# Optimization experiments

Hardware: AMD Instinct MI355X
Metric: run time of the kernel (lower is better)

Reference implementation:

```python
import jax, jax.numpy as jnp
import numpy as np

B, T, C, H = 4, 2048, 1024, 16
HD = C // H  # head dim = 64


def setup_inputs() -> dict:
    key = jax.random.key(0)
    k1, k2, k3 = jax.random.split(key, 3)
    scale_in = 1.0 / np.sqrt(C)
    return {
        "x": jax.random.normal(k1, (B, T, C), dtype=jnp.float32),
        "W_attn": jax.random.normal(k2, (C, 3 * C), dtype=jnp.float32) * scale_in,
        "b_attn": jnp.zeros((3 * C,), dtype=jnp.float32),
        "W_proj": jax.random.normal(k3, (C, C), dtype=jnp.float32) * scale_in,
        "b_proj": jnp.zeros((C,), dtype=jnp.float32),
    }


def reference(x, W_attn, b_attn, W_proj, b_proj):
    b, t, c = x.shape
    qkv = x @ W_attn + b_attn                      # [B,T,3C]
    q, k, v = jnp.split(qkv, 3, axis=-1)
    # [B,T,C] -> [B,H,T,HD]
    def heads(z):
        return z.reshape(b, t, H, HD).transpose(0, 2, 1, 3)
    q, k, v = heads(q), heads(k), heads(v)
    att = jnp.einsum("bhqd,bhkd->bhqk", q, k) / jnp.sqrt(jnp.float32(HD))
    causal = jnp.tril(jnp.ones((t, t), dtype=bool))
    att = jnp.where(causal, att, -jnp.inf)
    att = jax.nn.softmax(att, axis=-1)             # dropout p=0 -> identity
    y = jnp.einsum("bhqk,bhkd->bhqd", att, v)      # [B,H,T,HD]
    y = y.transpose(0, 2, 1, 3).reshape(b, t, c)   # [B,T,C]
    return y @ W_proj + b_proj
```

## Files before the change

kernel.cpp:

```cpp
#include <hip/hip_runtime.h>
#include <hip/hip_bf16.h>

typedef unsigned int u32;
typedef unsigned short u16;
typedef __bf16 bf16x8 __attribute__((ext_vector_type(8)));
typedef float f32x4 __attribute__((ext_vector_type(4)));
typedef _Float16 f16;
typedef _Float16 f16x2 __attribute__((ext_vector_type(2)));
typedef _Float16 f16x4 __attribute__((ext_vector_type(4)));
typedef _Float16 f16x8 __attribute__((ext_vector_type(8)));

#define B_ 4
#define T_ 2048
#define C_ 1024
#define H_ 16
#define HD_ 64
#define M_ (B_*T_)
#define N3C (3*C_)
#define N2C (2*C_)

__device__ __forceinline__ u16 f2bf(float f) {
  u32 u = __builtin_bit_cast(u32, f);
  u = (u + 0x7fffu + ((u >> 16) & 1u)) >> 16;
  return (u16)u;
}

#define GLD16(gp, lp) __builtin_amdgcn_global_load_lds( \
    (const __attribute__((address_space(1))) u32*)(gp), \
    (__attribute__((address_space(3))) u32*)(lp), 16, 0, 0)

#if __has_builtin(__builtin_amdgcn_exp2f)
#define EXP2F(x) __builtin_amdgcn_exp2f(x)
#else
#define EXP2F(x) exp2f(x)
#endif

template<int N> __device__ __forceinline__ void vmw() {
  if constexpr (N == 0)      asm volatile("s_waitcnt vmcnt(0)" ::: "memory");
  else if constexpr (N == 3) asm volatile("s_waitcnt vmcnt(3)" ::: "memory");
  else if constexpr (N == 4) asm volatile("s_waitcnt vmcnt(4)" ::: "memory");
  else if constexpr (N == 6) asm volatile("s_waitcnt vmcnt(6)" ::: "memory");
  else                       asm volatile("s_waitcnt vmcnt(8)" ::: "memory");
}

__global__ __launch_bounds__(256) void prep(
    const float* __restrict__ x, const float* __restrict__ Wa,
    const float* __restrict__ Wp,
    u16* __restrict__ xb, u16* __restrict__ W1t, u16* __restrict__ W2t) {
  __shared__ float t[32][33];
  const int blk = blockIdx.x, tid = threadIdx.x;
  if (blk < 8192) {
    int i = blk * 256 + tid;
    float4 v = ((const float4*)x)[i];
    ushort4 o;
    o.x = f2bf(v.x); o.y = f2bf(v.y); o.z = f2bf(v.z); o.w = f2bf(v.w);
    ((ushort4*)xb)[i] = o;
    return;
  }
  const float* W; u16* Wt; int Ndim, id;
  if (blk < 8192 + 3072) { W = Wa; Wt = W1t; Ndim = N3C; id = blk - 8192; }
  else                   { W = Wp; Wt = W2t; Ndim = C_;  id = blk - 11264; }
  const int nt = Ndim / 32;
  const int n0 = (id % nt) * 32, k0 = (id / nt) * 32;
  const int tx = tid & 31, ty = tid >> 5;
  #pragma unroll
  for (int i = ty; i < 32; i += 8)
    t[i][tx] = W[(long)(k0 + i) * Ndim + n0 + tx];
  __syncthreads();
  #pragma unroll
  for (int i = ty; i < 32; i += 8)
    Wt[(long)(n0 + i) * C_ + k0 + tx] = f2bf(t[tx][i]);
}

template<int BM>
__device__ __forceinline__ void gemm_core32(
    const u16* __restrict__ A, const u16* __restrict__ Bt,
    u16* lds, long rowA0, long colB0, int tid, f32x4 acc[BM/32][4]) {
  constexpr int MT = BM / 32;
  constexpr int SA = BM / 128;
  constexpr int AEL = BM * 32;
  constexpr int SLOTE = (BM + 256) * 32;
  constexpr int VMAIN = 2 * (SA + 2);
  const int lane = tid & 63, wave = tid >> 6;
  const int wm = wave >> 2, wn = wave & 3;
  const int l15 = lane & 15, quad = lane >> 4;
  const int srow = tid >> 2;
  const int schunk = (tid & 3) ^ (srow & 3);
  const u16* Ag = A + (long)(rowA0 + srow) * C_ + (schunk << 3);
  const u16* Bg = Bt + (long)(colB0 + srow) * C_ + (schunk << 3);
  const int fsw = (quad ^ (l15 & 3)) << 3;
  const int aOff = (wm * (BM / 2) + l15) * 32 + fsw;
  const int bOff = AEL + (wn * 64 + l15) * 32 + fsw;

#define SLOTP(k) (lds + ((k) & 3) * SLOTE)
#define STA_(k, j) GLD16(Ag + (k) * 32 + (long)(j) * 128 * C_, \
                         SLOTP(k) + (j) * 4096 + tid * 8)
#define STB_(k, j) GLD16(Bg + (k) * 32 + (long)(j) * 128 * C_, \
                         SLOTP(k) + AEL + (j) * 4096 + tid * 8)
#define KTILE_(kt, SC, WC) do {                                              \
    const u16* sl_ = SLOTP(kt);                                              \
    SC;                                                                      \
    bf16x8 bfr[4], afr[MT];                                                  \
    _Pragma("unroll")                                                        \
    for (int n = 0; n < 4; ++n)                                              \
      bfr[n] = *(const bf16x8*)&sl_[bOff + n * 512];                         \
    _Pragma("unroll")                                                        \
    for (int m = 0; m < MT; ++m)                                             \
      afr[m] = *(const bf16x8*)&sl_[aOff + m * 512];                         \
    asm volatile("s_waitcnt lgkmcnt(0)" ::: "memory");                       \
    __builtin_amdgcn_sched_barrier(0);                                       \
    __builtin_amdgcn_s_setprio(1);                                           \
    _Pragma("unroll")                                                        \
    for (int m = 0; m < MT; ++m)                                             \
      _Pragma("unroll")                                                      \
      for (int n = 0; n < 4; ++n)                                            \
        acc[m][n] = __builtin_amdgcn_mfma_f32_16x16x32_bf16(                 \
            afr[m], bfr[n], acc[m][n], 0, 0, 0);                             \
    __builtin_amdgcn_s_setprio(0);                                           \
    WC;                                                                      \
    asm volatile("s_barrier" ::: "memory");                                  \
  } while (0)

  #pragma unroll
  for (int t = 0; t < 3; ++t) {
    STA_(t, 0); STB_(t, 0); STB_(t, 1);
    if constexpr (SA == 2) STA_(t, 1);
  }
  vmw<VMAIN>();
  asm volatile("s_barrier" ::: "memory");

  #pragma unroll
  for (int kt = 0; kt < 29; ++kt) {
    KTILE_(kt,
           { STA_(kt + 3, 0); STB_(kt + 3, 0); STB_(kt + 3, 1);
             if constexpr (SA == 2) STA_(kt + 3, 1); },
           (vmw<VMAIN>()));
  }
  KTILE_(29, , (vmw<VMAIN / 2>()));
  KTILE_(30, , (vmw<0>()));
  KTILE_(31, , );
#undef KTILE_
#undef STB_
#undef STA_
#undef SLOTP
}

__global__ __launch_bounds__(512, 2) void gemm_qkv(
    const u16* __restrict__ A, const u16* __restrict__ Bt,
    const float* __restrict__ bias, u16* __restrict__ qkout,
    f16* __restrict__ vt) {
  __shared__ u16 lds[4 * 512 * 32];
  const int tid = threadIdx.x;
  const long rowA0 = (long)blockIdx.x * 256;
  const long colB0 = (long)blockIdx.y * 256;
  f32x4 acc[8][4] = {};
  gemm_core32<256>(A, Bt, lds, rowA0, colB0, tid, acc);

  const int lane = tid & 63, wave = tid >> 6;
  const int wm = wave >> 2, wn = wave & 3;
  const int l15 = lane & 15, quad = lane >> 4;
  float bl[4];
  #pragma unroll
  for (int nt = 0; nt < 4; ++nt)
    bl[nt] = bias[colB0 + wn * 64 + nt * 16 + l15];

  const bool vmode = (colB0 >= N2C);
  #pragma unroll
  for (int mt = 0; mt < 8; ++mt) {
    long row = rowA0 + wm * 128 + mt * 16 + quad * 4;
    #pragma unroll
    for (int nt = 0; nt < 4; ++nt) {
      long col = colB0 + wn * 64 + nt * 16 + l15;
      float v0 = acc[mt][nt][0] + bl[nt];
      float v1 = acc[mt][nt][1] + bl[nt];
      float v2 = acc[mt][nt][2] + bl[nt];
      float v3 = acc[mt][nt][3] + bl[nt];
      if (!vmode) {
        qkout[(row + 0) * N2C + col] = f2bf(v0);
        qkout[(row + 1) * N2C + col] = f2bf(v1);
        qkout[(row + 2) * N2C + col] = f2bf(v2);
        qkout[(row + 3) * N2C + col] = f2bf(v3);
      } else {
        int cv = (int)(col - N2C);
        int hh = cv >> 6, dd = cv & 63;
        int bb = (int)(row >> 11);
        long t = row & 2047;
        f16x2 lo = __builtin_bit_cast(f16x2, __builtin_amdgcn_cvt_pkrtz(v0, v1));
        f16x2 hi = __builtin_bit_cast(f16x2, __builtin_amdgcn_cvt_pkrtz(v2, v3));
        f16x4 w; w[0] = lo[0]; w[1] = lo[1]; w[2] = hi[0]; w[3] = hi[1];
        *(f16x4*)&vt[(((long)bb * H_ + hh) * HD_ + dd) * T_ + t] = w;
      }
    }
  }
}

__global__ __launch_bounds__(512, 2) void gemm_proj(
    const u16* __restrict__ A, const u16* __restrict__ Bt,
    const float* __restrict__ bias, float* __restrict__ Cout) {
  __shared__ u16 lds[4 * 384 * 32];
  const int tid = threadIdx.x;
  const long rowA0 = (long)blockIdx.x * 128;
  const long colB0 = (long)blockIdx.y * 256;
  f32x4 acc[4][4] = {};
  gemm_core32<128>(A, Bt, lds, rowA0, colB0, tid, acc);

  const int lane = tid & 63, wave = tid >> 6;
  const int wm = wave >> 2, wn = wave & 3;
  const int l15 = lane & 15, quad = lane >> 4;
  float bl[4];
  #pragma unroll
  for (int nt = 0; nt < 4; ++nt)
    bl[nt] = bias[colB0 + wn * 64 + nt * 16 + l15];
  #pragma unroll
  for (int mt = 0; mt < 4; ++mt) {
    long row = rowA0 + wm * 64 + mt * 16 + quad * 4;
    #pragma unroll
    for (int nt = 0; nt < 4; ++nt) {
      long col = colB0 + wn * 64 + nt * 16 + l15;
      #pragma unroll
      for (int r = 0; r < 4; ++r)
        Cout[(row + r) * C_ + col] = acc[mt][nt][r] + bl[nt];
    }
  }
}

__global__ __launch_bounds__(256, 5) void flash_attn(
    const u16* __restrict__ qk, const f16* __restrict__ vt,
    u16* __restrict__ yb) {
  __shared__ u16 KsF[2 * 64 * 64];
  __shared__ f16 VsF[2 * 64 * 64];
  const int l = blockIdx.x;
  const int bh = l & 63;
  const int qt = 31 - (l >> 6);
  const int b = bh >> 4, h = bh & 15;
  const int tid = threadIdx.x, wave = tid >> 6, lane = tid & 63;
  const int l15 = lane & 15, quad = lane >> 4;
  const int rA = lane >> 3, cxor = (lane & 7) ^ rA;
  const int c2 = lane & 7;

  const u16* Qb = qk + (long)b * T_ * N2C + h * HD_;
  const f16* Vbase = vt + (long)bh * HD_ * T_;
  const u16* Kb0 = Qb + C_ + (long)(wave * 16 + rA) * N2C + cxor * 8;
  const f16* Vb0 = Vbase + (long)(wave * 16 + rA) * T_ + c2 * 8;

  u16* ksw0 = &KsF[(wave * 16) * 64];
  u16* ksw1 = &KsF[4096 + (wave * 16) * 64];

  const int blkA = 4 * (c2 & 1) + (c2 >> 2);
  const int subO = ((c2 >> 1) & 1) * 4;
  const int rowW = (wave * 16 + rA) * 64;
  const int wvA = rowW + ((blkA ^ rA) << 3) + subO;
  const int wvB = rowW + (((blkA + 2) ^ rA) << 3) + subO;

  const int kA0 = l15 * 64 + ((quad ^ (l15 & 3)) << 3) + (((l15 >> 2) & 1) << 5);
  const int kA1 = kA0 ^ 32;
  const int vR0 = l15 * 64 + ((((quad * 2) ^ (l15 & 7))) << 3);

  const float cs = 0.125f * 1.44269504088896340736f;

#define VLO(v) __builtin_shufflevector(v, v, 0, 1, 2, 3)
#define VHI(v) __builtin_shufflevector(v, v, 4, 5, 6, 7)
#define WRV(bo, a0, a1) do {                                                   \
    *(f16x4*)&VsF[(bo) + wvA] = VLO(a0);                                       \
    *(f16x4*)&VsF[(bo) + wvB] = VHI(a0);                                       \
    *(f16x4*)&VsF[(bo) + wvA + 512] = VLO(a1);                                 \
    *(f16x4*)&VsF[(bo) + wvB + 512] = VHI(a1);                                 \
  } while (0)

#define FA_TILE(KT, BUF) do {                                                  \
    __syncthreads();             \
    f16x8 vr0, vr1;                                                            \
    const bool pre_ = (KT) + 1 < nKT;                                          \
    if (pre_) {                                                                \
      vr0 = *(const f16x8*)vp;                   \
      vr1 = *(const f16x8*)(vp + 8 * T_);                                      \
      u16* kd = (BUF) ? ksw0 : ksw1;                                           \
      GLD16(kp, kd);                                                           \
      GLD16(kp + 8 * N2C, kd + 8 * 64);                                        \
      kp += 64 * N2C;                                                          \
      vp += 64;                                                                \
    }                                                                          \
    f32x4 St[4] = {};                                                          \
    __builtin_amdgcn_s_setprio(1);                                             \
    _Pragma("unroll")                                                          \
    for (int kk = 0; kk < 2; ++kk) {                                           \
      bf16x8 qf = kk ? bq1 : bq0;                                              \
      const int ki = ((kk ? kA1 : kA0)) + (BUF) * 4096;                        \
      _Pragma("unroll")                                                        \
      for (int mt = 0; mt < 4; ++mt) {                                         \
        bf16x8 kf = *(const bf16x8*)&KsF[ki + mt * 1024];                      \
        St[mt] = __builtin_amdgcn_mfma_f32_16x16x32_bf16(kf, qf, St[mt],       \
                                                         0, 0, 0);             \
      }                                                                        \
    }                                                                          \
    __builtin_amdgcn_s_setprio(0);                                             \
    if ((KT) == qt) {                                                          \
      _Pragma("unroll")                                                        \
      for (int mt = 0; mt < 4; ++mt)                                           \
        _Pragma("unroll")                                                      \
        for (int r = 0; r < 4; ++r)                                            \
          if (mt * 16 + quad * 4 + r > wave * 16 + l15)                        \
            St[mt][r] = -__builtin_inff();                                     \
    }                                                                          \
    if (pre_) { WRV((BUF) ? 0 : 4096, vr0, vr1); }       \
    float ps = 0.f;                                                            \
    f16x4 pf[4];                                                               \
    _Pragma("unroll")                                                          \
    for (int mt = 0; mt < 4; ++mt) {                                           \
      float p0 = EXP2F(__builtin_fmaf(St[mt][0], cs, nref));                   \
      float p1 = EXP2F(__builtin_fmaf(St[mt][1], cs, nref));                   \
      float p2 = EXP2F(__builtin_fmaf(St[mt][2], cs, nref));                   \
      float p3 = EXP2F(__builtin_fmaf(St[mt][3], cs, nref));                   \
      ps += (p0 + p1) + (p2 + p3);                                             \
      f16x2 lo = __builtin_bit_cast(f16x2, __builtin_amdgcn_cvt_pkrtz(p0, p1));\
      f16x2 hi = __builtin_bit_cast(f16x2, __builtin_amdgcn_cvt_pkrtz(p2, p3));\
      pf[mt][0] = lo[0]; pf[mt][1] = lo[1];                                    \
      pf[mt][2] = hi[0]; pf[mt][3] = hi[1];                                    \
    }                                                                          \
    li += ps;                                                                  \
    __builtin_amdgcn_s_setprio(1);                                             \
    _Pragma("unroll")                                                          \
    for (int j = 0; j < 2; ++j) {                                              \
      const int vi = (vR0 ^ (j << 3)) + (BUF) * 4096;                          \
      _Pragma("unroll")                                                        \
      for (int dt = 0; dt < 4; ++dt) {                                         \
        f16x8 vv = *(const f16x8*)&VsF[vi + dt * 1024];                        \
        o[dt] = __builtin_amdgcn_mfma_f32_16x16x16f16(VLO(vv), pf[2 * j],      \
                                                      o[dt], 0, 0, 0);         \
        o[dt] = __builtin_amdgcn_mfma_f32_16x16x16f16(VHI(vv), pf[2 * j + 1],  \
                                                      o[dt], 0, 0, 0);         \
      }                                                                        \
    }                                                                          \
    __builtin_amdgcn_s_setprio(0);                                             \
  } while (0)

  const int nKT = qt + 1;
  const int qrow = qt * 64 + wave * 16 + l15;
  const bf16x8 bq0 = *(const bf16x8*)&Qb[(long)qrow * N2C + quad * 8];
  const bf16x8 bq1 = *(const bf16x8*)&Qb[(long)qrow * N2C + 32 + quad * 8];

  float qq = 0.f;
  #pragma unroll
  for (int j = 0; j < 8; ++j) {
    float a = (float)bq0[j], bv = (float)bq1[j];
    qq = __builtin_fmaf(a, a, qq);
    qq = __builtin_fmaf(bv, bv, qq);
  }
  qq += __shfl_xor(qq, 16);
  qq += __shfl_xor(qq, 32);
  const float nref = -qq * cs;

  const u16* kp = Kb0;
  const f16* vp = Vb0;

  {
    f16x8 a0 = *(const f16x8*)vp;
    f16x8 a1 = *(const f16x8*)(vp + 8 * T_);
    GLD16(kp, ksw0);
    GLD16(kp + 8 * N2C, ksw0 + 8 * 64);
    kp += 64 * N2C;
    vp += 64;
    WRV(0, a0, a1);
  }

  float li = 0.f;
  f32x4 o[4] = {};

  int kt = 0;
  #pragma unroll 1
  for (; kt + 1 < nKT; kt += 2) {
    FA_TILE(kt, 0);
    FA_TILE(kt + 1, 1);
  }
  if (nKT & 1) FA_TILE(nKT - 1, 0);

  li += __shfl_xor(li, 16);
  li += __shfl_xor(li, 32);
  float inv = 1.f / li;
  #pragma unroll
  for (int dt = 0; dt < 4; ++dt) {
    ushort4 w;
    w.x = f2bf(o[dt][0] * inv);
    w.y = f2bf(o[dt][1] * inv);
    w.z = f2bf(o[dt][2] * inv);
    w.w = f2bf(o[dt][3] * inv);
    *(ushort4*)&yb[((long)b * T_ + qrow) * C_ + h * HD_ + dt * 16 + quad * 4] = w;
  }
#undef FA_TILE
#undef WRV
#undef VHI
#undef VLO
}

extern "C" void kernel_launch(void* const* d_in, const int* in_sizes, int n_in,
                              void* d_out, int out_size, void* d_ws, size_t ws_size,
                              hipStream_t stream) {
  const float* x      = (const float*)d_in[0];
  const float* W_attn = (const float*)d_in[1];
  const float* b_attn = (const float*)d_in[2];
  const float* W_proj = (const float*)d_in[3];
  const float* b_proj = (const float*)d_in[4];
  float* out = (float*)d_out;

  char* ws = (char*)d_ws;
  u16* xb   = (u16*)(ws);
  u16* W1t  = (u16*)(ws + 16777216);
  u16* W2t  = (u16*)(ws + 23068672);
  u16* qkb  = (u16*)(ws + 25165824);
  f16* vtb  = (f16*)(ws + 58720256);
  u16* yb   = (u16*)(ws + 75497472);

  prep<<<dim3(12288), dim3(256), 0, stream>>>(x, W_attn, W_proj, xb, W1t, W2t);
  gemm_qkv<<<dim3(M_ / 256, N3C / 256), dim3(512), 0, stream>>>(
      xb, W1t, b_attn, qkb, vtb);
  flash_attn<<<dim3(2048), dim3(256), 0, stream>>>(qkb, vtb, yb);
  gemm_proj<<<dim3(M_ / 128, C_ / 256), dim3(512), 0, stream>>>(
      yb, W2t, b_proj, out);
}
```

Measured before the change: 241.3 us.

## Double-buffer GEMM LDS fragments in registers and split MFMA into halves

Restructures the shared GEMM core so that each K-tile's MFMA work runs in two halves. While the second half runs, the B fragments and first-half A fragments for the next tile are read from LDS into registers, so LDS read latency overlaps with matrix math. The global-to-LDS load issue is split across the two halves. The vmcnt wait is tightened to leave only one tile outstanding. The LDS XOR swizzle also changes to use bits 1-2 of the row, which is meant to cut bank conflicts. In exchange it uses more VGPRs for the next-tile fragments and register copies, which could hurt occupancy at 2 blocks per CU.

After: 237.1 us. About the same (-1.7%).

```diff
diff --git a/kernel.cpp b/kernel.cpp
--- a/kernel.cpp
+++ b/kernel.cpp
@@ -41,6 +41,13 @@
   else if constexpr (N == 4) asm volatile("s_waitcnt vmcnt(4)" ::: "memory");
   else if constexpr (N == 6) asm volatile("s_waitcnt vmcnt(6)" ::: "memory");
   else                       asm volatile("s_waitcnt vmcnt(8)" ::: "memory");
+}
+template<int N> __device__ __forceinline__ void lgw() {
+  if constexpr (N == 0)      asm volatile("s_waitcnt lgkmcnt(0)" ::: "memory");
+  else if constexpr (N == 2) asm volatile("s_waitcnt lgkmcnt(2)" ::: "memory");
+  else if constexpr (N == 4) asm volatile("s_waitcnt lgkmcnt(4)" ::: "memory");
+  else if constexpr (N == 6) asm volatile("s_waitcnt lgkmcnt(6)" ::: "memory");
+  else                       asm volatile("s_waitcnt lgkmcnt(8)" ::: "memory");
 }
 
 __global__ __launch_bounds__(256) void prep(
@@ -77,69 +84,99 @@
     const u16* __restrict__ A, const u16* __restrict__ Bt,
     u16* lds, long rowA0, long colB0, int tid, f32x4 acc[BM/32][4]) {
   constexpr int MT = BM / 32;
+  constexpr int MH = MT / 2;
   constexpr int SA = BM / 128;
+  constexpr int L  = SA + 2;
   constexpr int AEL = BM * 32;
   constexpr int SLOTE = (BM + 256) * 32;
-  constexpr int VMAIN = 2 * (SA + 2);
   const int lane = tid & 63, wave = tid >> 6;
   const int wm = wave >> 2, wn = wave & 3;
   const int l15 = lane & 15, quad = lane >> 4;
   const int srow = tid >> 2;
-  const int schunk = (tid & 3) ^ (srow & 3);
+  const int schunk = (tid & 3) ^ ((tid >> 3) & 3);
   const u16* Ag = A + (long)(rowA0 + srow) * C_ + (schunk << 3);
   const u16* Bg = Bt + (long)(colB0 + srow) * C_ + (schunk << 3);
-  const int fsw = (quad ^ (l15 & 3)) << 3;
+  const int fsw = (quad ^ ((l15 >> 1) & 3)) << 3;
   const int aOff = (wm * (BM / 2) + l15) * 32 + fsw;
   const int bOff = AEL + (wn * 64 + l15) * 32 + fsw;
+
+  bf16x8 aC[MT], bC[4], aN[MH], bN[4];
 
 #define SLOTP(k) (lds + ((k) & 3) * SLOTE)
 #define STA_(k, j) GLD16(Ag + (k) * 32 + (long)(j) * 128 * C_, \
                          SLOTP(k) + (j) * 4096 + tid * 8)
 #define STB_(k, j) GLD16(Bg + (k) * 32 + (long)(j) * 128 * C_, \
                          SLOTP(k) + AEL + (j) * 4096 + tid * 8)
-#define KTILE_(kt, SC, WC) do {                                              \
-    const u16* sl_ = SLOTP(kt);                                              \
-    SC;                                                                      \
-    bf16x8 bfr[4], afr[MT];                                                  \
+#define MMH_(h) do {                                                         \
     _Pragma("unroll")                                                        \
-    for (int n = 0; n < 4; ++n)                                              \
-      bfr[n] = *(const bf16x8*)&sl_[bOff + n * 512];                         \
+    for (int m = 0; m < MH; ++m)                                             \
+      _Pragma("unroll")                                                      \
+      for (int n = 0; n < 4; ++n)                                            \
+        acc[(h) * MH + m][n] = __builtin_amdgcn_mfma_f32_16x16x32_bf16(      \
+            aC[(h) * MH + m], bC[n], acc[(h) * MH + m][n], 0, 0, 0);         \
+  } while (0)
+#define KTILE_(kt, S1, S2, RA, WC) do {                                      \
+                                                      \
     _Pragma("unroll")                                                        \
-    for (int m = 0; m < MT; ++m)                                             \
-      afr[m] = *(const bf16x8*)&sl_[aOff + m * 512];                         \
-    asm volatile("s_waitcnt lgkmcnt(0)" ::: "memory");                       \
+    for (int m = 0; m < MH; ++m)                                             \
+      aC[MH + m] = *(const bf16x8*)&SLOTP(kt)[aOff + (MH + m) * 512];        \
+    S1;                                                                      \
+    lgw<MH>();                                                               \
     __builtin_amdgcn_sched_barrier(0);                                       \
     __builtin_amdgcn_s_setprio(1);                                           \
-    _Pragma("unroll")                                                        \
-    for (int m = 0; m < MT; ++m)                                             \
+    MMH_(0);                                                                 \
+    __builtin_amdgcn_s_setprio(0);                                           \
+                                                      \
+    if constexpr (RA) {                                                      \
       _Pragma("unroll")                                                      \
       for (int n = 0; n < 4; ++n)                                            \
-        acc[m][n] = __builtin_amdgcn_mfma_f32_16x16x32_bf16(                 \
-            afr[m], bfr[n], acc[m][n], 0, 0, 0);                             \
+        bN[n] = *(const bf16x8*)&SLOTP((kt) + 1)[bOff + n * 512];            \
+      _Pragma("unroll")                                                      \
+      for (int m = 0; m < MH; ++m)                                           \
+        aN[m] = *(const bf16x8*)&SLOTP((kt) + 1)[aOff + m * 512];            \
+    }                                                                        \
+    S2;                                                                      \
+    lgw<(RA) ? (4 + MH) : 0>();                                              \
+    __builtin_amdgcn_sched_barrier(0);                                       \
+    __builtin_amdgcn_s_setprio(1);                                           \
+    MMH_(1);                                                                 \
     __builtin_amdgcn_s_setprio(0);                                           \
     WC;                                                                      \
     asm volatile("s_barrier" ::: "memory");                                  \
+    if constexpr (RA) {                                                      \
+      _Pragma("unroll")                                                      \
+      for (int n = 0; n < 4; ++n) bC[n] = bN[n];                             \
+      _Pragma("unroll")                                                      \
+      for (int m = 0; m < MH; ++m) aC[m] = aN[m];                            \
+    }                                                                        \
   } while (0)
 
   #pragma unroll
   for (int t = 0; t < 3; ++t) {
-    STA_(t, 0); STB_(t, 0); STB_(t, 1);
-    if constexpr (SA == 2) STA_(t, 1);
-  }
-  vmw<VMAIN>();
+    STA_(t, 0); if constexpr (SA == 2) STA_(t, 1);
+    STB_(t, 0); STB_(t, 1);
+  }
+  vmw<L>();
   asm volatile("s_barrier" ::: "memory");
+  #pragma unroll
+  for (int n = 0; n < 4; ++n)
+    bC[n] = *(const bf16x8*)&SLOTP(0)[bOff + n * 512];
+  #pragma unroll
+  for (int m = 0; m < MH; ++m)
+    aC[m] = *(const bf16x8*)&SLOTP(0)[aOff + m * 512];
 
   #pragma unroll
   for (int kt = 0; kt < 29; ++kt) {
     KTILE_(kt,
-           { STA_(kt + 3, 0); STB_(kt + 3, 0); STB_(kt + 3, 1);
-             if constexpr (SA == 2) STA_(kt + 3, 1); },
-           (vmw<VMAIN>()));
-  }
-  KTILE_(29, , (vmw<VMAIN / 2>()));
-  KTILE_(30, , (vmw<0>()));
-  KTILE_(31, , );
+           { STA_(kt + 3, 0); STB_(kt + 3, 0); },
+           { if constexpr (SA == 2) STA_(kt + 3, 1); STB_(kt + 3, 1); },
+           1, (vmw<L>()));
+  }
+  KTILE_(29, , , 1, (vmw<0>()));
+  KTILE_(30, , , 1, );
+  KTILE_(31, , , 0, );
 #undef KTILE_
+#undef MMH_
 #undef STB_
 #undef STA_
 #undef SLOTP
```
